# Optimization experiments

Hardware: AMD Instinct MI355X
Metric: run time of the kernel (lower is better)

Reference implementation:

```python
import jax, jax.numpy as jnp
import numpy as np

D_MODEL = 1024
NUM_HEADS = 16
NUM_KV_HEADS = 4
D_K = D_MODEL // NUM_HEADS              # 64
G = NUM_HEADS // NUM_KV_HEADS           # queries per kv head = 4
B, S = 2, 2048


def setup_inputs() -> dict:
    key = jax.random.key(0)
    ks = jax.random.split(key, 11)
    s = 0.02
    return {
        "query": jax.random.normal(ks[0], (B, S, D_MODEL), jnp.float32),
        "key_in": jax.random.normal(ks[1], (B, S, D_MODEL), jnp.float32),
        "value_in": jax.random.normal(ks[2], (B, S, D_MODEL), jnp.float32),
        "Wq": jax.random.normal(ks[3], (D_MODEL, D_MODEL), jnp.float32) * s,
        "bq": jnp.zeros((D_MODEL,), jnp.float32),
        "Wk": jax.random.normal(ks[4], (D_MODEL, NUM_KV_HEADS * D_K), jnp.float32) * s,
        "bk": jnp.zeros((NUM_KV_HEADS * D_K,), jnp.float32),
        "Wv": jax.random.normal(ks[5], (D_MODEL, NUM_KV_HEADS * D_K), jnp.float32) * s,
        "bv": jnp.zeros((NUM_KV_HEADS * D_K,), jnp.float32),
        "Wo": jax.random.normal(ks[6], (D_MODEL, D_MODEL), jnp.float32) * s,
        "bo": jnp.zeros((D_MODEL,), jnp.float32),
    }


def reference(query, key_in, value_in, Wq, bq, Wk, bk, Wv, bv, Wo, bo):
    scale = jnp.sqrt(jnp.asarray(D_K, query.dtype))
    # Projections
    Q = (query @ Wq + bq).reshape(B, S, NUM_HEADS, D_K).transpose(0, 2, 1, 3)        # [B,H,S,dk]
    K = (key_in @ Wk + bk).reshape(B, S, NUM_KV_HEADS, D_K).transpose(0, 2, 1, 3)    # [B,KVH,S,dk]
    V = (value_in @ Wv + bv).reshape(B, S, NUM_KV_HEADS, D_K).transpose(0, 2, 1, 3)  # [B,KVH,S,dk]
    # repeat_interleave over head dim -> group Q heads by KV head instead
    Qg = Q.reshape(B, NUM_KV_HEADS, G, S, D_K)                                       # [B,KVH,G,S,dk]
    scores = jnp.einsum('bkgqd,bksd->bkgqs', Qg, K) / scale                          # [B,KVH,G,S,S]
    attn = jax.nn.softmax(scores, axis=-1)
    ctx = jnp.einsum('bkgqs,bksd->bkgqd', attn, V)                                   # [B,KVH,G,S,dk]
    ctx = ctx.reshape(B, NUM_HEADS, S, D_K).transpose(0, 2, 1, 3).reshape(B, S, D_MODEL)
    output = ctx @ Wo + bo
    # new_cache: K[:, ::G] on the repeated tensor == original K/V per kv head
    return output, K, V
```

## Files before the change

### kernel.cpp

```cpp
#include <hip/hip_runtime.h>

typedef unsigned short u16;
typedef unsigned int u32;
typedef __attribute__((ext_vector_type(8))) short short8;
typedef __attribute__((ext_vector_type(4))) float f32x4;

#define MFMA16(a, b, c) __builtin_amdgcn_mfma_f32_16x16x32_bf16(a, b, c, 0, 0, 0)

#define SEQ 2048
#define DM 1024

__device__ __forceinline__ u16 f2bf(float f) {
  u32 u = __float_as_uint(f);
  u += 0x7fffu + ((u >> 16) & 1u);
  return (u16)(u >> 16);
}
__device__ __forceinline__ u32 pack2(float a, float b) {
  u32 r;
  asm("v_cvt_pk_bf16_f32 %0, %1, %2" : "=v"(r) : "v"(a), "v"(b));
  return r;
}
__device__ __forceinline__ u32 pack2t(float a, float b) {
  return __builtin_amdgcn_perm(__float_as_uint(b), __float_as_uint(a), 0x07060302u);
}
__device__ __forceinline__ uint4 cvt8(const float* f) {
  float4 a = *(const float4*)f;
  float4 b = *(const float4*)(f + 4);
  uint4 r;
  r.x = pack2(a.x, a.y);
  r.y = pack2(a.z, a.w);
  r.z = pack2(b.x, b.y);
  r.w = pack2(b.z, b.w);
  return r;
}
__device__ __forceinline__ void gload16(const u16* g, u16* l) {
  __builtin_amdgcn_global_load_lds((const __attribute__((address_space(1))) u32*)g,
                                   (__attribute__((address_space(3))) u32*)l, 16, 0, 0);
}

__global__ void k_tr(const float* __restrict__ Wq, const float* __restrict__ Wk,
                     const float* __restrict__ Wv, const float* __restrict__ Wo,
                     u16* __restrict__ WqT, u16* __restrict__ WkT, u16* __restrict__ WvT,
                     u16* __restrict__ WoT) {
  const int z = blockIdx.z;
  const float* W = z == 0 ? Wq : (z == 1 ? Wk : (z == 2 ? Wv : Wo));
  u16* Wt = z == 0 ? WqT : (z == 1 ? WkT : (z == 2 ? WvT : WoT));
  const int N = (z == 1 || z == 2) ? 256 : 1024;
  const int n0 = blockIdx.x * 32;
  if (n0 >= N) return;
  const int k0 = blockIdx.y * 32;
  __shared__ float tile[32][33];
  int x = threadIdx.x & 31, y = threadIdx.x >> 5;
#pragma unroll
  for (int i = 0; i < 4; i++)
    tile[y + i * 8][x] = W[(size_t)(k0 + y + i * 8) * N + n0 + x];
  __syncthreads();
#pragma unroll
  for (int i = 0; i < 4; i++)
    Wt[(size_t)(n0 + y + i * 8) * 1024 + k0 + x] = f2bf(tile[x][y + i * 8]);
}

template <bool A32, bool B32>
__device__ __forceinline__ void gemm64(const void* __restrict__ A, const void* __restrict__ Bt,
                                       int m0, int n0, u16* lA, u16* lB, f32x4 acc[2][4]) {
  const int tid = threadIdx.x;
  const int lane = tid & 63, wave = tid >> 6;
  const int l15 = lane & 15, quad = lane >> 4;
  const int wm = wave >> 1, wn = wave & 1;
  const int sr = tid >> 3, scol = (tid & 7) * 8;
  f32x4 zero = {0.f, 0.f, 0.f, 0.f};
#pragma unroll
  for (int i = 0; i < 2; i++)
#pragma unroll
    for (int j = 0; j < 4; j++) acc[i][j] = zero;

  for (int k0 = 0; k0 < 1024; k0 += 64) {
    if constexpr (A32) {
      const float* Af = (const float*)A;
#pragma unroll
      for (int it = 0; it < 2; it++) {
        int r = sr + it * 32;
        uint4 v = cvt8(Af + (size_t)(m0 + r) * 1024 + k0 + scol);
        *(uint4*)&lA[r * 64 + (((tid & 7) ^ (r & 7)) << 3)] = v;
      }
    } else {
      const u16* Ab = (const u16*)A;
#pragma unroll
      for (int it = 0; it < 2; it++) {
        int w8 = wave * 2 + it;
        int r = w8 * 8 + (lane >> 3);
        int g = (lane & 7) ^ (lane >> 3);
        gload16(Ab + (size_t)(m0 + r) * 1024 + k0 + g * 8, &lA[w8 * 512]);
      }
    }
    if constexpr (B32) {
      const float* Bf = (const float*)Bt;
#pragma unroll
      for (int it = 0; it < 4; it++) {
        int r = sr + it * 32;
        uint4 v = cvt8(Bf + (size_t)(n0 + r) * 1024 + k0 + scol);
        *(uint4*)&lB[r * 64 + (((tid & 7) ^ (r & 7)) << 3)] = v;
      }
    } else {
      const u16* Bb = (const u16*)Bt;
#pragma unroll
      for (int it = 0; it < 4; it++) {
        int w8 = wave * 4 + it;
        int r = w8 * 8 + (lane >> 3);
        int g = (lane & 7) ^ (lane >> 3);
        gload16(Bb + (size_t)(n0 + r) * 1024 + k0 + g * 8, &lB[w8 * 512]);
      }
    }
    __syncthreads();
    short8 af[2][2], bfr[4][2];
#pragma unroll
    for (int i = 0; i < 2; i++)
#pragma unroll
      for (int kb = 0; kb < 2; kb++) {
        int r = wm * 32 + i * 16 + l15;
        af[i][kb] = *(const short8*)&lA[r * 64 + (((kb * 4 + quad) ^ (r & 7)) << 3)];
      }
#pragma unroll
    for (int j = 0; j < 4; j++)
#pragma unroll
      for (int kb = 0; kb < 2; kb++) {
        int r = wn * 64 + j * 16 + l15;
        bfr[j][kb] = *(const short8*)&lB[r * 64 + (((kb * 4 + quad) ^ (r & 7)) << 3)];
      }
#pragma unroll
    for (int i = 0; i < 2; i++)
#pragma unroll
      for (int j = 0; j < 4; j++) {
        acc[i][j] = MFMA16(af[i][0], bfr[j][0], acc[i][j]);
        acc[i][j] = MFMA16(af[i][1], bfr[j][1], acc[i][j]);
      }
    __syncthreads();
  }
}

__global__ __launch_bounds__(256) void k_proj(
    const float* __restrict__ query, const float* __restrict__ key_in,
    const float* __restrict__ value_in, const u16* __restrict__ WqT,
    const u16* __restrict__ WkT, const u16* __restrict__ WvT, const float* __restrict__ bq,
    const float* __restrict__ bk, const float* __restrict__ bv, u16* __restrict__ qbf,
    float* __restrict__ outK, u16* __restrict__ kbf, float* __restrict__ outV,
    u16* __restrict__ vtb, float qscale) {
  __shared__ u16 lA[64 * 64];
  __shared__ u16 lB[128 * 64];
  const int idx = blockIdx.x;
  const int lane = threadIdx.x & 63, wave = threadIdx.x >> 6;
  const int l15 = lane & 15, quad = lane >> 4;
  const int wm = wave >> 1, wn = wave & 1;
  f32x4 acc[2][4];

  if (idx < 640) {
    const u16* Wt;
    const float* act;
    const float* bias;
    int m0, n0, mode;
    if (idx < 512) {
      Wt = WqT; act = query; bias = bq; m0 = (idx >> 5) * 64; n0 = (idx & 31) * 128; mode = 0;
    } else {
      int i2 = idx - 512;
      Wt = WkT; act = key_in; bias = bk; m0 = (i2 >> 5) * 64; n0 = (i2 & 31) * 128; mode = 1;
    }
    gemm64<false, true>(Wt, act, m0, n0, lA, lB, acc);
#pragma unroll
    for (int i = 0; i < 2; i++) {
      int c0 = m0 + wm * 32 + i * 16 + quad * 4;
      float4 bb = *(const float4*)(bias + c0);
#pragma unroll
      for (int j = 0; j < 4; j++) {
        int token = n0 + wn * 64 + j * 16 + l15;
        int b = token >> 11, s = token & 2047;
        float v0 = acc[i][j][0] + bb.x, v1 = acc[i][j][1] + bb.y;
        float v2 = acc[i][j][2] + bb.z, v3 = acc[i][j][3] + bb.w;
        int d = c0 & 63;
        if (mode == 0) {
          int h = c0 >> 6;
          uint2 o;
          o.x = pack2(v0 * qscale, v1 * qscale);
          o.y = pack2(v2 * qscale, v3 * qscale);
          *(uint2*)(qbf + (((size_t)(b * 16 + h) * SEQ + s) << 6) + d) = o;
        } else {
          int kvh = c0 >> 6;
          size_t ix = (((size_t)(b * 4 + kvh) * SEQ + s) << 6) + d;
          float4 vv = {v0, v1, v2, v3};
          *(float4*)(outK + ix) = vv;
          uint2 o;
          o.x = pack2(v0, v1);
          o.y = pack2(v2, v3);
          *(uint2*)(kbf + ix) = o;
        }
      }
    }
  } else {
    int i2 = idx - 640;
    int m0 = (i2 >> 1) * 64, n0 = (i2 & 1) * 128;
    gemm64<true, false>(value_in, WvT, m0, n0, lA, lB, acc);
#pragma unroll
    for (int i = 0; i < 2; i++) {
      int r0 = m0 + wm * 32 + i * 16 + quad * 4;
      int b = r0 >> 11, s0 = r0 & 2047;
#pragma unroll
      for (int j = 0; j < 4; j++) {
        int col = n0 + wn * 64 + j * 16 + l15;
        int kvh = col >> 6, d = col & 63;
        float bv_ = bv[col];
        float v0 = acc[i][j][0] + bv_, v1 = acc[i][j][1] + bv_;
        float v2 = acc[i][j][2] + bv_, v3 = acc[i][j][3] + bv_;
        size_t base = (((size_t)(b * 4 + kvh) * SEQ + s0) << 6) + d;
        outV[base] = v0;
        outV[base + 64] = v1;
        outV[base + 128] = v2;
        outV[base + 192] = v3;
        uint2 o;
        o.x = pack2(v0, v1);
        o.y = pack2(v2, v3);
        *(uint2*)(vtb + ((size_t)(b * 4 + kvh) * 64 + d) * SEQ + s0) = o;
      }
    }
  }
}

__global__ __launch_bounds__(256) void k_out(const u16* __restrict__ ctxb,
                                             const u16* __restrict__ WoT,
                                             const float* __restrict__ bo,
                                             float* __restrict__ out) {
  __shared__ u16 lA[64 * 64];
  __shared__ u16 lB[128 * 64];
  const int idx = blockIdx.x;
  const int m0 = (idx >> 5) * 64, n0 = (idx & 31) * 128;
  const int lane = threadIdx.x & 63, wave = threadIdx.x >> 6;
  const int l15 = lane & 15, quad = lane >> 4;
  const int wm = wave >> 1, wn = wave & 1;
  f32x4 acc[2][4];
  gemm64<false, false>(WoT, ctxb, m0, n0, lA, lB, acc);
#pragma unroll
  for (int i = 0; i < 2; i++) {
    int c0 = m0 + wm * 32 + i * 16 + quad * 4;
    float4 bb = *(const float4*)(bo + c0);
#pragma unroll
    for (int j = 0; j < 4; j++) {
      int token = n0 + wn * 64 + j * 16 + l15;
      float4 vv = {acc[i][j][0] + bb.x, acc[i][j][1] + bb.y, acc[i][j][2] + bb.z,
                   acc[i][j][3] + bb.w};
      *(float4*)(out + (size_t)token * DM + c0) = vv;
    }
  }
}

__global__ __launch_bounds__(256, 2) void k_flash(const u16* __restrict__ Qh,
                                                  const u16* __restrict__ Kb,
                                                  const u16* __restrict__ Vt,
                                                  u16* __restrict__ ctx) {
  __shared__ u16 lK[128 * 64];
  __shared__ u16 lV[64 * 128];
  __shared__ u16 lP[4 * 32 * 64];
  const int tid = threadIdx.x;
  const int lane = tid & 63, wave = tid >> 6;
  const int l15 = lane & 15, quad = lane >> 4;
  const int bh = blockIdx.y;
  const int b = bh >> 4, h = bh & 15, kvh = h >> 2;
  const u16* Q = Qh + (size_t)bh * SEQ * 64;
  const u16* Kp = Kb + (size_t)(b * 4 + kvh) * SEQ * 64;
  const u16* Vp = Vt + (size_t)(b * 4 + kvh) * 64 * SEQ;
  const int q0 = blockIdx.x * 128 + wave * 32;

  short8 qf[2][2];
#pragma unroll
  for (int g = 0; g < 2; g++)
#pragma unroll
    for (int kb = 0; kb < 2; kb++)
      qf[g][kb] = *(const short8*)(Q + (size_t)(q0 + g * 16 + l15) * 64 + kb * 32 + quad * 8);

  short8 ones8;
  {
    short ov = (l15 == 0) ? (short)0x3F80 : (short)0;
    ones8 = (short8){ov, ov, ov, ov, ov, ov, ov, ov};
  }

  f32x4 zero = {0.f, 0.f, 0.f, 0.f};
  f32x4 acc[2][4];
  f32x4 lacc[2] = {zero, zero};
#pragma unroll
  for (int g = 0; g < 2; g++)
#pragma unroll
    for (int n = 0; n < 4; n++) acc[g][n] = zero;

  u16* lPw = lP + wave * (32 * 64);
  const int gr3 = lane >> 3, gc7 = lane & 7;
  const int gr4 = lane >> 4, gc15 = lane & 15;

  for (int kc = 0; kc < SEQ; kc += 128) {
    __syncthreads();
#pragma unroll
    for (int i = 0; i < 4; i++) {
      int slab = wave * 4 + i;
      gload16(Kp + (size_t)(kc + slab * 8 + gr3) * 64 + ((gc7 ^ gr3) << 3), lK + slab * 512);
    }
#pragma unroll
    for (int i = 0; i < 4; i++) {
      int slab = wave * 4 + i;
      int row = slab * 4 + gr4;
      gload16(Vp + (size_t)row * SEQ + kc + ((gc15 ^ (row & 15)) << 3), lV + slab * 512);
    }
    __syncthreads();

#pragma unroll
    for (int sub = 0; sub < 2; sub++) {
      const int ks = sub * 64;
      f32x4 sc[2][4];
#pragma unroll
      for (int mt = 0; mt < 4; mt++) {
        int row = ks + mt * 16 + l15;
        short8 kf0 = *(const short8*)&lK[row * 64 + ((quad ^ (row & 7)) << 3)];
        short8 kf1 = *(const short8*)&lK[row * 64 + (((4 + quad) ^ (row & 7)) << 3)];
#pragma unroll
        for (int g = 0; g < 2; g++) {
          f32x4 t = MFMA16(kf0, qf[g][0], zero);
          sc[g][mt] = MFMA16(kf1, qf[g][1], t);
        }
      }
#pragma unroll
      for (int g = 0; g < 2; g++)
#pragma unroll
        for (int mt = 0; mt < 4; mt++) {
          float e0 = __builtin_amdgcn_exp2f(sc[g][mt][0]);
          float e1 = __builtin_amdgcn_exp2f(sc[g][mt][1]);
          float e2 = __builtin_amdgcn_exp2f(sc[g][mt][2]);
          float e3 = __builtin_amdgcn_exp2f(sc[g][mt][3]);
          int chp = mt * 2 + (quad >> 1);
          uint2 p;
          p.x = pack2t(e0, e1);
          p.y = pack2t(e2, e3);
          *(uint2*)&lPw[(g * 16 + l15) * 64 + ((chp ^ (l15 & 7)) << 3) + (quad & 1) * 4] = p;
        }
      __asm__ volatile("s_waitcnt lgkmcnt(0)" ::: "memory");
#pragma unroll
      for (int kbp = 0; kbp < 2; kbp++) {
        int chq = kbp * 4 + quad;
        short8 pf0 = *(const short8*)&lPw[l15 * 64 + ((chq ^ (l15 & 7)) << 3)];
        short8 pf1 = *(const short8*)&lPw[(16 + l15) * 64 + ((chq ^ (l15 & 7)) << 3)];
        lacc[0] = MFMA16(ones8, pf0, lacc[0]);
        lacc[1] = MFMA16(ones8, pf1, lacc[1]);
#pragma unroll
        for (int n = 0; n < 4; n++) {
          int row = n * 16 + l15;
          int chv = sub * 8 + kbp * 4 + quad;
          short8 vf = *(const short8*)&lV[row * 128 + ((chv ^ (row & 15)) << 3)];
          acc[0][n] = MFMA16(vf, pf0, acc[0][n]);
          acc[1][n] = MFMA16(vf, pf1, acc[1][n]);
        }
      }
    }
  }

#pragma unroll
  for (int g = 0; g < 2; g++) {
    float lq = __shfl(lacc[g][0], l15);
    float inv = __builtin_amdgcn_rcpf(lq);
    u16* base = ctx + ((size_t)(b * SEQ + q0 + g * 16 + l15)) * DM + h * 64;
#pragma unroll
    for (int n = 0; n < 4; n++) {
      uint2 o;
      o.x = pack2t(acc[g][n][0] * inv, acc[g][n][1] * inv);
      o.y = pack2t(acc[g][n][2] * inv, acc[g][n][3] * inv);
      *(uint2*)(base + n * 16 + quad * 4) = o;
    }
  }
}

extern "C" void kernel_launch(void* const* d_in, const int* in_sizes, int n_in,
                              void* d_out, int out_size, void* d_ws, size_t ws_size,
                              hipStream_t stream) {
  const float* query = (const float*)d_in[0];
  const float* key_in = (const float*)d_in[1];
  const float* value_in = (const float*)d_in[2];
  const float* Wq = (const float*)d_in[3];
  const float* bq = (const float*)d_in[4];
  const float* Wk = (const float*)d_in[5];
  const float* bk = (const float*)d_in[6];
  const float* Wv = (const float*)d_in[7];
  const float* bv = (const float*)d_in[8];
  const float* Wo = (const float*)d_in[9];
  const float* bo = (const float*)d_in[10];

  float* out = (float*)d_out;
  float* outK = out + 4194304;
  float* outV = out + 5242880;

  char* ws = (char*)d_ws;
  u16* WqT = (u16*)(ws);
  u16* WkT = (u16*)(ws + 2097152);
  u16* WvT = (u16*)(ws + 2621440);
  u16* WoT = (u16*)(ws + 3145728);
  u16* qbf = (u16*)(ws + 5242880);
  u16* kbf = (u16*)(ws + 13631488);
  u16* vtb = (u16*)(ws + 15728640);
  u16* ctxb = (u16*)(ws + 17825792);

  const float qscale = 0.125f * 1.44269504088896340736f;

  k_tr<<<dim3(32, 32, 4), 256, 0, stream>>>(Wq, Wk, Wv, Wo, WqT, WkT, WvT, WoT);
  k_proj<<<dim3(768), 256, 0, stream>>>(query, key_in, value_in, WqT, WkT, WvT, bq, bk, bv,
                                        qbf, outK, kbf, outV, vtb, qscale);
  k_flash<<<dim3(16, 32), 256, 0, stream>>>(qbf, kbf, vtb, ctxb);
  k_out<<<dim3(512), 256, 0, stream>>>(ctxb, WoT, bo, out);
}
```

Measured before the change: 205.5 us.

## Double-buffer K/V tiles and keep P in registers via permlane swaps

Splits the K/V LDS staging into two buffers so the next tile's global-to-LDS loads are issued before computing on the current tile, with one barrier per iteration instead of two. It also drops the per-wave LDS round trip for the probability matrix. The exp'd scores are packed to bf16 and rearranged into MFMA operand layout with v_permlane32/16_swap. The cost is doubled LDS for K/V, which may affect occupancy. It also relies on the permlane swap sequence producing exactly the layout the old LDS transpose did.

Measured after the change: 200.1 us, median of 2. -2.7%, faster.

```diff
diff --git a/kernel.cpp b/kernel.cpp
--- a/kernel.cpp
+++ b/kernel.cpp
@@ -22,6 +22,12 @@
 }
 __device__ __forceinline__ u32 pack2t(float a, float b) {
   return __builtin_amdgcn_perm(__float_as_uint(b), __float_as_uint(a), 0x07060302u);
+}
+__device__ __forceinline__ void pswap32(u32& a, u32& b) {
+  asm("v_permlane32_swap_b32 %0, %1" : "+v"(a), "+v"(b));
+}
+__device__ __forceinline__ void pswap16(u32& a, u32& b) {
+  asm("v_permlane16_swap_b32 %0, %1" : "+v"(a), "+v"(b));
 }
 __device__ __forceinline__ uint4 cvt8(const float* f) {
   float4 a = *(const float4*)f;
@@ -254,9 +260,8 @@
                                                   const u16* __restrict__ Kb,
                                                   const u16* __restrict__ Vt,
                                                   u16* __restrict__ ctx) {
-  __shared__ u16 lK[128 * 64];
-  __shared__ u16 lV[64 * 128];
-  __shared__ u16 lP[4 * 32 * 64];
+  __shared__ u16 lK[2][128 * 64];
+  __shared__ u16 lV[2][64 * 128];
   const int tid = threadIdx.x;
   const int lane = tid & 63, wave = tid >> 6;
   const int l15 = lane & 15, quad = lane >> 4;
@@ -288,24 +293,32 @@
 #pragma unroll
     for (int n = 0; n < 4; n++) acc[g][n] = zero;
 
-  u16* lPw = lP + wave * (32 * 64);
   const int gr3 = lane >> 3, gc7 = lane & 7;
   const int gr4 = lane >> 4, gc15 = lane & 15;
 
-  for (int kc = 0; kc < SEQ; kc += 128) {
-    __syncthreads();
+  auto stage = [&](int kc, int bufi) {
+    u16* dK = lK[bufi];
+    u16* dV = lV[bufi];
 #pragma unroll
     for (int i = 0; i < 4; i++) {
       int slab = wave * 4 + i;
-      gload16(Kp + (size_t)(kc + slab * 8 + gr3) * 64 + ((gc7 ^ gr3) << 3), lK + slab * 512);
+      gload16(Kp + (size_t)(kc + slab * 8 + gr3) * 64 + ((gc7 ^ gr3) << 3), dK + slab * 512);
     }
 #pragma unroll
     for (int i = 0; i < 4; i++) {
       int slab = wave * 4 + i;
       int row = slab * 4 + gr4;
-      gload16(Vp + (size_t)row * SEQ + kc + ((gc15 ^ (row & 15)) << 3), lV + slab * 512);
-    }
-    __syncthreads();
+      gload16(Vp + (size_t)row * SEQ + kc + ((gc15 ^ (row & 15)) << 3), dV + slab * 512);
+    }
+  };
+
+  stage(0, 0);
+  __syncthreads();
+
+  for (int t = 0; t < SEQ / 128; t++) {
+    if (t < SEQ / 128 - 1) stage((t + 1) * 128, (t + 1) & 1);
+    const u16* cK = lK[t & 1];
+    const u16* cV = lV[t & 1];
 
 #pragma unroll
     for (int sub = 0; sub < 2; sub++) {
@@ -314,46 +327,50 @@
 #pragma unroll
       for (int mt = 0; mt < 4; mt++) {
         int row = ks + mt * 16 + l15;
-        short8 kf0 = *(const short8*)&lK[row * 64 + ((quad ^ (row & 7)) << 3)];
-        short8 kf1 = *(const short8*)&lK[row * 64 + (((4 + quad) ^ (row & 7)) << 3)];
+        short8 kf0 = *(const short8*)&cK[row * 64 + ((quad ^ (row & 7)) << 3)];
+        short8 kf1 = *(const short8*)&cK[row * 64 + (((4 + quad) ^ (row & 7)) << 3)];
 #pragma unroll
         for (int g = 0; g < 2; g++) {
-          f32x4 t = MFMA16(kf0, qf[g][0], zero);
-          sc[g][mt] = MFMA16(kf1, qf[g][1], t);
+          f32x4 t0 = MFMA16(kf0, qf[g][0], zero);
+          sc[g][mt] = MFMA16(kf1, qf[g][1], t0);
         }
       }
 #pragma unroll
       for (int g = 0; g < 2; g++)
 #pragma unroll
-        for (int mt = 0; mt < 4; mt++) {
-          float e0 = __builtin_amdgcn_exp2f(sc[g][mt][0]);
-          float e1 = __builtin_amdgcn_exp2f(sc[g][mt][1]);
-          float e2 = __builtin_amdgcn_exp2f(sc[g][mt][2]);
-          float e3 = __builtin_amdgcn_exp2f(sc[g][mt][3]);
-          int chp = mt * 2 + (quad >> 1);
-          uint2 p;
-          p.x = pack2t(e0, e1);
-          p.y = pack2t(e2, e3);
-          *(uint2*)&lPw[(g * 16 + l15) * 64 + ((chp ^ (l15 & 7)) << 3) + (quad & 1) * 4] = p;
+        for (int mt = 0; mt < 4; mt++)
+#pragma unroll
+          for (int r = 0; r < 4; r++) sc[g][mt][r] = __builtin_amdgcn_exp2f(sc[g][mt][r]);
+
+#pragma unroll
+      for (int kbp = 0; kbp < 2; kbp++) {
+        short8 pf[2];
+#pragma unroll
+        for (int g = 0; g < 2; g++) {
+          u32 U0 = pack2t(sc[g][2 * kbp][0], sc[g][2 * kbp][1]);
+          u32 W0 = pack2t(sc[g][2 * kbp + 1][0], sc[g][2 * kbp + 1][1]);
+          u32 U1 = pack2t(sc[g][2 * kbp][2], sc[g][2 * kbp][3]);
+          u32 W1 = pack2t(sc[g][2 * kbp + 1][2], sc[g][2 * kbp + 1][3]);
+          pswap32(U0, W0);
+          pswap16(U0, W0);
+          pswap32(U1, W1);
+          pswap16(U1, W1);
+          u32 w[4] = {U0, U1, W0, W1};
+          pf[g] = *(const short8*)w;
         }
-      __asm__ volatile("s_waitcnt lgkmcnt(0)" ::: "memory");
-#pragma unroll
-      for (int kbp = 0; kbp < 2; kbp++) {
-        int chq = kbp * 4 + quad;
-        short8 pf0 = *(const short8*)&lPw[l15 * 64 + ((chq ^ (l15 & 7)) << 3)];
-        short8 pf1 = *(const short8*)&lPw[(16 + l15) * 64 + ((chq ^ (l15 & 7)) << 3)];
-        lacc[0] = MFMA16(ones8, pf0, lacc[0]);
-        lacc[1] = MFMA16(ones8, pf1, lacc[1]);
+        lacc[0] = MFMA16(ones8, pf[0], lacc[0]);
+        lacc[1] = MFMA16(ones8, pf[1], lacc[1]);
 #pragma unroll
         for (int n = 0; n < 4; n++) {
           int row = n * 16 + l15;
           int chv = sub * 8 + kbp * 4 + quad;
-          short8 vf = *(const short8*)&lV[row * 128 + ((chv ^ (row & 15)) << 3)];
-          acc[0][n] = MFMA16(vf, pf0, acc[0][n]);
-          acc[1][n] = MFMA16(vf, pf1, acc[1][n]);
+          short8 vf = *(const short8*)&cV[row * 128 + ((chv ^ (row & 15)) << 3)];
+          acc[0][n] = MFMA16(vf, pf[0], acc[0][n]);
+          acc[1][n] = MFMA16(vf, pf[1], acc[1][n]);
         }
       }
     }
+    __syncthreads();
   }
 
 #pragma unroll
```
